# Kernel tuning notes

Measured on AMD Instinct MI355X. Metric: run time of the kernel, lower is better.

Reference implementation:

```python
import jax, jax.numpy as jnp
import numpy as np

V_NUM = 4
NUM_HEADS = 8


def setup_inputs() -> dict:
    key = jax.random.key(0)
    k1, k2, k3 = jax.random.split(key, 3)
    B, C, H, W = 8, 512, 24, 24
    x = jax.random.normal(k1, (B, C, H, W), dtype=jnp.float32)
    # 1x1 conv weights stored as [out_ch, in_ch]
    w_qkv = jax.random.normal(k2, (3 * C, C), dtype=jnp.float32) * (C ** -0.5)
    w_proj = jax.random.normal(k3, (C, C), dtype=jnp.float32) * (C ** -0.5)
    b_proj = jnp.zeros((C,), dtype=jnp.float32)
    return {"x": x, "w_qkv": w_qkv, "w_proj": w_proj, "b_proj": b_proj}


def reference(x, w_qkv, w_proj, b_proj):
    B, C, H, W = x.shape
    hd = C // NUM_HEADS          # head dim
    scale = hd ** -0.5
    g = B // V_NUM               # batch groups
    N = V_NUM * H * W            # tokens per group

    # 1x1 conv qkv (no bias): [B, 3C, H, W]
    qkv = jnp.einsum('bchw,oc->bohw', x, w_qkv)
    # [g, v, 3C, H, W] -> [g, 3C, v, H, W] -> [g, heads, 3*hd, N]
    t = qkv.reshape(g, V_NUM, 3 * C, H, W).transpose(0, 2, 1, 3, 4)
    t = t.reshape(g, NUM_HEADS, 3 * hd, N)
    q, k, v = jnp.split(t, 3, axis=2)  # each [g, heads, hd, N]

    # attn = k^T @ q * scale : [g, heads, N, N]
    attn = jnp.einsum('ghdn,ghdm->ghnm', k, q) * scale
    attn = jax.nn.softmax(attn, axis=-2)  # softmax over the k axis (dim=-2)

    # out = v @ attn : [g, heads, hd, N]
    out = jnp.einsum('ghdn,ghnm->ghdm', v, attn)
    # [g, C, v, H, W] -> [g, v, C, H, W] -> [B, C, H, W]
    out = out.reshape(g, C, V_NUM, H, W).transpose(0, 2, 1, 3, 4).reshape(B, C, H, W)

    # 1x1 conv proj with bias
    out = jnp.einsum('bchw,oc->bohw', out, w_proj) + b_proj[None, :, None, None]
    return out
```

## Files before the change

kernel.cpp:

```cpp
#include <hip/hip_runtime.h>
#include <stdint.h>

typedef _Float16 f16;
typedef _Float16 half8 __attribute__((ext_vector_type(8)));
typedef _Float16 half4 __attribute__((ext_vector_type(4)));
typedef float floatx4 __attribute__((ext_vector_type(4)));

#define LOG2E 1.44269504088896340736f

__device__ __forceinline__ void async_cp16(const void* g, void* l) {
  __builtin_amdgcn_global_load_lds((const __attribute__((address_space(1))) void*)g,
                                   (__attribute__((address_space(3))) void*)l, 16, 0, 0);
}

__global__ __launch_bounds__(256) void k_prep(const float* __restrict__ x,
                                              f16* __restrict__ XT,
                                              const float* __restrict__ wqkv,
                                              const float* __restrict__ wproj,
                                              f16* __restrict__ WQ, f16* __restrict__ WP) {
  __shared__ f16 sT[64][72];
  const int bid = blockIdx.x;
  const int tid = threadIdx.x;
  if (bid < 576) {
    const int hw0 = (bid % 9) * 64, c0 = ((bid / 9) & 7) * 64, b = bid / 72;
    const int cc = tid >> 6, hwc = tid & 63;
    const float* xb = x + (size_t)b * 294912;
    for (int i = 0; i < 16; ++i) {
      int c = c0 + i * 4 + cc;
      sT[hwc][i * 4 + cc] = (f16)xb[c * 576 + hw0 + hwc];
    }
    __syncthreads();
    const int c_c = tid & 63, rr = tid >> 6;
    f16* xtb = XT + ((size_t)b * 576 + hw0) * 512 + c0;
    for (int j = 0; j < 16; ++j) {
      int r = j * 4 + rr;
      xtb[(size_t)r * 512 + c_c] = sT[r][c_c];
    }
  } else {
    const float SCALE_Q = 0.125f * LOG2E;
    const int total1 = 1536 * 512, total2 = 512 * 512;
    for (int idx = (bid - 576) * 256 + tid; idx < total1 + total2; idx += 128 * 256) {
      if (idx < total1) {
        int row = idx >> 9;
        float v = wqkv[idx];
        if ((row % 192) < 64) v *= SCALE_Q;
        WQ[idx] = (f16)v;
      } else {
        WP[idx - total1] = (f16)wproj[idx - total1];
      }
    }
  }
}

__global__ __launch_bounds__(256) void k_qkv_gemm(const f16* __restrict__ XT,
                                                  const f16* __restrict__ WQ,
                                                  f16* __restrict__ Qh, f16* __restrict__ Kh,
                                                  f16* __restrict__ Vh) {
  const int t0 = blockIdx.x * 128, n0 = blockIdx.y * 128;
  __shared__ alignas(16) f16 smem[2 * 128 * 64];
  f16* sA = smem;
  f16* sB = smem + 128 * 64;
  const int tid = threadIdx.x;
  const int wave = tid >> 6, lane = tid & 63, quad = lane >> 4, l16 = lane & 15;
  const int msub = (wave & 1) * 64, nsub = (wave >> 1) * 64;
  const floatx4 fzero = {0.f, 0.f, 0.f, 0.f};
  floatx4 acc[4][4];
  for (int i = 0; i < 4; ++i)
    for (int j = 0; j < 4; ++j) acc[i][j] = fzero;

  for (int k0 = 0; k0 < 512; k0 += 64) {
    __syncthreads();
    for (int p = 0; p < 4; ++p) {
      int e = p * 256 + tid;
      int row = e >> 3, colb = e & 7;
      async_cp16((const char*)XT + ((size_t)(t0 + row) * 512 + k0 + colb * 8) * 2,
                 (char*)sA + e * 16);
      async_cp16((const char*)WQ + ((size_t)(n0 + row) * 512 + k0 + colb * 8) * 2,
                 (char*)sB + e * 16);
    }
    __syncthreads();
    for (int f = 0; f < 2; ++f) {
      half8 a[4], bfr[4];
      for (int ms = 0; ms < 4; ++ms)
        a[ms] = *(const half8*)&sA[(msub + ms * 16 + l16) * 64 + f * 32 + quad * 8];
      for (int ns = 0; ns < 4; ++ns)
        bfr[ns] = *(const half8*)&sB[(nsub + ns * 16 + l16) * 64 + f * 32 + quad * 8];
      for (int ms = 0; ms < 4; ++ms)
        for (int ns = 0; ns < 4; ++ns)
          acc[ms][ns] =
              __builtin_amdgcn_mfma_f32_16x16x32_f16(a[ms], bfr[ns], acc[ms][ns], 0, 0, 0);
    }
  }
  for (int ms = 0; ms < 4; ++ms) {
    int tbase = t0 + msub + ms * 16 + quad * 4;
    for (int ns = 0; ns < 4; ++ns) {
      int row = n0 + nsub + ns * 16 + l16;
      int h = row / 192, rr2 = row % 192;
      int sel = rr2 >> 6, d = rr2 & 63;
      if (sel == 2) continue;
      for (int r = 0; r < 4; ++r) {
        int t = tbase + r;
        int b = t / 576, hw = t % 576;
        int g = b >> 2, v = b & 3;
        int n = v * 576 + hw;
        int gh = g * 8 + h;
        f16 hv = (f16)acc[ms][ns][r];
        size_t idx = ((size_t)gh * 2304 + n) * 64 + d;
        if (sel == 0)
          Qh[idx] = hv;
        else
          Kh[idx] = hv;
      }
    }
  }
  const int r0 = n0 % 192;
  if (r0 != 0) {
    const int vloc = (r0 == 128) ? 0 : 64;
    const int h = (n0 + vloc) / 192;
    f16* sVT = smem;
    __syncthreads();
    if ((wave >> 1) == (vloc >> 6)) {
      for (int ms = 0; ms < 4; ++ms) {
        int tok = msub + ms * 16 + quad * 4;
        for (int ns = 0; ns < 4; ++ns) {
          int d = ns * 16 + l16;
          half4 hv;
          for (int r = 0; r < 4; ++r) hv[r] = (f16)acc[ms][ns][r];
          *(half4*)&sVT[d * 136 + tok] = hv;
        }
      }
    }
    __syncthreads();
    for (int pss = 0; pss < 4; ++pss) {
      int d = pss * 16 + (tid >> 4), chunk = tid & 15;
      int t = t0 + chunk * 8;
      int b = t / 576, hw = t - b * 576;
      int gh = (b >> 2) * 8 + h, n = (b & 3) * 576 + hw;
      *(half8*)(Vh + (size_t)gh * 147456 + (size_t)d * 2304 + n) =
          *(const half8*)&sVT[d * 136 + chunk * 8];
    }
  }
}

__global__ __launch_bounds__(384) void k_attn(const f16* __restrict__ Qh,
                                              const f16* __restrict__ Kh,
                                              const f16* __restrict__ Vh,
                                              f16* __restrict__ AOT) {
  const int mt = blockIdx.x, gh = blockIdx.y;
  const int m0 = mt * 48;
  const int g = gh >> 3, h = gh & 7;
  const f16* Qg = Qh + (size_t)gh * 147456;
  const f16* Kg = Kh + (size_t)gh * 147456;
  const f16* Vg = Vh + (size_t)gh * 147456;
  __shared__ alignas(16) f16 smem[16384];
  f16* sK = smem;
  f16* sV = smem + 8192;
  const int tid = threadIdx.x;
  const int wave = tid >> 6, lane = tid & 63, quad = lane >> 4, l16 = lane & 15;
  const int str = wave & 1, qgrp = wave >> 1;
  const floatx4 fzero = {0.f, 0.f, 0.f, 0.f};
  const int sw = l16 & 7;
  const int vsw = (l16 >> 1) & 3;

  auto stage_kv = [&](int ktile, int buf) {
#pragma unroll
    for (int p = 0; p < 3; ++p) {
      int idx = p * 384 + tid;
      if (idx < 1024) {
        int isV = idx >= 512;
        int rem = idx & 511;
        int st = rem >> 8, unit = rem & 255;
        if (!isV) {
          int row = unit >> 3, cb = unit & 7;
          async_cp16(
              Kg + (size_t)(st * 1152 + ktile * 32 + row) * 64 + ((cb ^ (row & 7)) << 3),
              (char*)(sK + (st * 2 + buf) * 2048) + unit * 16);
        } else {
          int row = unit >> 2, cb = unit & 3;
          async_cp16(Vg + (size_t)row * 2304 + st * 1152 + ktile * 32 +
                         ((cb ^ ((row >> 1) & 3)) << 3),
                     (char*)(sV + (st * 2 + buf) * 2048) + unit * 16);
        }
      }
    }
  };

  half8 qa[2];
  {
    int qrow = m0 + qgrp * 16 + l16;
    qa[0] = *(const half8*)(Qg + (size_t)qrow * 64 + quad * 8);
    qa[1] = *(const half8*)(Qg + (size_t)qrow * 64 + 32 + quad * 8);
  }

  stage_kv(0, 0);
  __syncthreads();
  stage_kv(1, 1);

  float l_lane = 0.f;
  floatx4 o[4];
  for (int dt = 0; dt < 4; ++dt) o[dt] = fzero;

  for (int kt = 0; kt < 36; ++kt) {
    const f16* bK = sK + (str * 2 + (kt & 1)) * 2048;
    const f16* bV = sV + (str * 2 + (kt & 1)) * 2048;

    half4 pf[2];
#pragma unroll
    for (int nt = 0; nt < 2; ++nt) {
      int krow = nt * 16 + l16;
      half8 kb0 = *(const half8*)&bK[krow * 64 + ((quad ^ sw) << 3)];
      half8 kb1 = *(const half8*)&bK[krow * 64 + (((4 + quad) ^ sw) << 3)];
      floatx4 t = __builtin_amdgcn_mfma_f32_16x16x32_f16(kb0, qa[0], fzero, 0, 0, 0);
      t = __builtin_amdgcn_mfma_f32_16x16x32_f16(kb1, qa[1], t, 0, 0, 0);
#pragma unroll
      for (int r = 0; r < 4; ++r) {
        float e = __builtin_amdgcn_exp2f(t[r]);
        l_lane += e;
        pf[nt][r] = (f16)e;
      }
    }
#pragma unroll
    for (int dt = 0; dt < 4; ++dt) {
      int vrow = dt * 16 + l16;
#pragma unroll
      for (int nt = 0; nt < 2; ++nt) {
        int chunk = nt * 2 + (quad >> 1);
        half4 vb = *(const half4*)&bV[vrow * 32 + ((chunk ^ vsw) << 3) + (quad & 1) * 4];
        o[dt] = __builtin_amdgcn_mfma_f32_16x16x16f16(pf[nt], vb, o[dt], 0, 0, 0);
      }
    }

    if (kt < 35) {
      __syncthreads();
      if (kt + 2 < 36) stage_kv(kt + 2, kt & 1);
    }
  }

  __syncthreads();
  float* cO = (float*)smem;
  float* cL = (float*)(smem + 8192);
  if (str == 1) {
    cL[qgrp * 64 + lane] = l_lane;
#pragma unroll
    for (int dt = 0; dt < 4; ++dt)
      *(floatx4*)&cO[((qgrp * 4 + dt) * 64 + lane) * 4] = o[dt];
  }
  __syncthreads();
  if (str == 0) {
    l_lane += cL[qgrp * 64 + lane];
#pragma unroll
    for (int dt = 0; dt < 4; ++dt)
      o[dt] += *(const floatx4*)&cO[((qgrp * 4 + dt) * 64 + lane) * 4];

    l_lane += __shfl_xor(l_lane, 16, 64);
    l_lane += __shfl_xor(l_lane, 32, 64);
    float inv[4];
#pragma unroll
    for (int r = 0; r < 4; ++r) {
      float lr = __shfl(l_lane, quad * 4 + r, 64);
      inv[r] = 1.f / lr;
    }
#pragma unroll
    for (int dt = 0; dt < 4; ++dt)
#pragma unroll
      for (int r = 0; r < 4; ++r) {
        int n_tok = m0 + qgrp * 16 + quad * 4 + r;
        int v = n_tok / 576, hw = n_tok % 576;
        int bb = g * 4 + v;
        int c = h * 64 + dt * 16 + l16;
        AOT[((size_t)bb * 576 + hw) * 512 + c] = (f16)(o[dt][r] * inv[r]);
      }
  }
}

__global__ __launch_bounds__(256) void k_proj_gemm(const f16* __restrict__ AOT,
                                                   const f16* __restrict__ WP,
                                                   const float* __restrict__ bias,
                                                   float* __restrict__ out) {
  const int o0 = blockIdx.x * 64, t0 = blockIdx.y * 128;
  __shared__ alignas(16) f16 sA[64 * 64];
  __shared__ alignas(16) f16 sB[128 * 64];
  const int tid = threadIdx.x;
  const int wave = tid >> 6, lane = tid & 63, quad = lane >> 4, l16 = lane & 15;
  const int msub = (wave & 1) * 32, nsub = (wave >> 1) * 64;
  const floatx4 fzero = {0.f, 0.f, 0.f, 0.f};
  floatx4 acc[2][4];
  for (int i = 0; i < 2; ++i)
    for (int j = 0; j < 4; ++j) acc[i][j] = fzero;

  for (int k0 = 0; k0 < 512; k0 += 64) {
    __syncthreads();
    for (int p = 0; p < 2; ++p) {
      int e = p * 256 + tid;
      int row = e >> 3, colb = e & 7;
      async_cp16((const char*)WP + ((size_t)(o0 + row) * 512 + k0 + colb * 8) * 2,
                 (char*)sA + e * 16);
    }
    for (int p = 0; p < 4; ++p) {
      int e = p * 256 + tid;
      int row = e >> 3, colb = e & 7;
      async_cp16((const char*)AOT + ((size_t)(t0 + row) * 512 + k0 + colb * 8) * 2,
                 (char*)sB + e * 16);
    }
    __syncthreads();
    for (int f = 0; f < 2; ++f) {
      half8 a[2], bfr[4];
      for (int ms = 0; ms < 2; ++ms)
        a[ms] = *(const half8*)&sA[(msub + ms * 16 + l16) * 64 + f * 32 + quad * 8];
      for (int ns = 0; ns < 4; ++ns)
        bfr[ns] = *(const half8*)&sB[(nsub + ns * 16 + l16) * 64 + f * 32 + quad * 8];
      for (int ms = 0; ms < 2; ++ms)
        for (int ns = 0; ns < 4; ++ns)
          acc[ms][ns] =
              __builtin_amdgcn_mfma_f32_16x16x32_f16(a[ms], bfr[ns], acc[ms][ns], 0, 0, 0);
    }
  }
  for (int ms = 0; ms < 2; ++ms) {
    int o_row = o0 + msub + ms * 16 + quad * 4;
    for (int ns = 0; ns < 4; ++ns) {
      int t = t0 + nsub + ns * 16 + l16;
      int b = t / 576, hw = t % 576;
      for (int r = 0; r < 4; ++r) {
        int orow = o_row + r;
        out[(size_t)b * 294912 + (size_t)orow * 576 + hw] = acc[ms][ns][r] + bias[orow];
      }
    }
  }
}

extern "C" void kernel_launch(void* const* d_in, const int* in_sizes, int n_in,
                              void* d_out, int out_size, void* d_ws, size_t ws_size,
                              hipStream_t stream) {
  const float* x = (const float*)d_in[0];
  const float* wqkv = (const float*)d_in[1];
  const float* wproj = (const float*)d_in[2];
  const float* bias = (const float*)d_in[3];
  float* out = (float*)d_out;
  char* ws = (char*)d_ws;
  f16* XT = (f16*)(ws + 0);
  f16* WQ = (f16*)(ws + 4718592);
  f16* WP = (f16*)(ws + 6291456);
  f16* Qh = (f16*)(ws + 6815744);
  f16* Kh = (f16*)(ws + 11534336);
  f16* Vh = (f16*)(ws + 16252928);
  f16* AOT = (f16*)(ws + 20971520);

  k_prep<<<dim3(704), dim3(256), 0, stream>>>(x, XT, wqkv, wproj, WQ, WP);
  k_qkv_gemm<<<dim3(36, 12), dim3(256), 0, stream>>>(XT, WQ, Qh, Kh, Vh);
  k_attn<<<dim3(48, 16), dim3(384), 0, stream>>>(Qh, Kh, Vh, AOT);
  k_proj_gemm<<<dim3(8, 36), dim3(256), 0, stream>>>(AOT, WP, bias, out);
}
```

Measured before the change: 148.0 us.

## Interleave V layout and load V directly from global into 16x16x32 MFMA

The V-producing kernel now writes V in an interleaved token order so that each lane can read a contiguous half8 of V straight from global memory. The attention kernel drops LDS staging for V, halves its shared memory, and raises launch bounds to ask for more resident blocks. The two P tiles are packed into one half8 so the PV product uses 16x16x32 MFMAs instead of pairs of 16x16x16. The exp results are converted with packed round-toward-zero and summed with fdot2. The risk is that direct global V loads expose latency that the async LDS pipeline used to hide, and the cL offset now depends on the reduced shared-memory layout.

```diff
diff --git a/kernel.cpp b/kernel.cpp
--- a/kernel.cpp
+++ b/kernel.cpp
@@ -4,6 +4,7 @@
 typedef _Float16 f16;
 typedef _Float16 half8 __attribute__((ext_vector_type(8)));
 typedef _Float16 half4 __attribute__((ext_vector_type(4)));
+typedef _Float16 half2 __attribute__((ext_vector_type(2)));
 typedef float floatx4 __attribute__((ext_vector_type(4)));
 
 #define LOG2E 1.44269504088896340736f
@@ -11,6 +12,10 @@
 __device__ __forceinline__ void async_cp16(const void* g, void* l) {
   __builtin_amdgcn_global_load_lds((const __attribute__((address_space(1))) void*)g,
                                    (__attribute__((address_space(3))) void*)l, 16, 0, 0);
+}
+
+__device__ __forceinline__ half2 pkrtz(float a, float b) {
+  return __builtin_bit_cast(half2, __builtin_amdgcn_cvt_pkrtz(a, b));
 }
 
 __global__ __launch_bounds__(256) void k_prep(const float* __restrict__ x,
@@ -132,55 +137,48 @@
     }
     __syncthreads();
     for (int pss = 0; pss < 4; ++pss) {
-      int d = pss * 16 + (tid >> 4), chunk = tid & 15;
-      int t = t0 + chunk * 8;
+      int d = pss * 16 + (tid >> 4);
+      int sub = tid & 15, gg = sub >> 2, u = sub & 3;
+      int t = t0 + gg * 32;
       int b = t / 576, hw = t - b * 576;
-      int gh = (b >> 2) * 8 + h, n = (b & 3) * 576 + hw;
-      *(half8*)(Vh + (size_t)gh * 147456 + (size_t)d * 2304 + n) =
-          *(const half8*)&sVT[d * 136 + chunk * 8];
-    }
-  }
-}
-
-__global__ __launch_bounds__(384) void k_attn(const f16* __restrict__ Qh,
-                                              const f16* __restrict__ Kh,
-                                              const f16* __restrict__ Vh,
-                                              f16* __restrict__ AOT) {
+      int gh = (b >> 2) * 8 + h, nb = (b & 3) * 576 + hw;
+      half4 va = *(const half4*)&sVT[d * 136 + gg * 32 + u * 4];
+      half4 vb2 = *(const half4*)&sVT[d * 136 + gg * 32 + 16 + u * 4];
+      half8 w = __builtin_shufflevector(va, vb2, 0, 4, 1, 5, 2, 6, 3, 7);
+      *(half8*)(Vh + (size_t)gh * 147456 + (size_t)d * 2304 + nb + u * 8) = w;
+    }
+  }
+}
+
+__global__ __launch_bounds__(384, 8) void k_attn(const f16* __restrict__ Qh,
+                                                 const f16* __restrict__ Kh,
+                                                 const f16* __restrict__ Vh,
+                                                 f16* __restrict__ AOT) {
   const int mt = blockIdx.x, gh = blockIdx.y;
   const int m0 = mt * 48;
   const int g = gh >> 3, h = gh & 7;
   const f16* Qg = Qh + (size_t)gh * 147456;
   const f16* Kg = Kh + (size_t)gh * 147456;
   const f16* Vg = Vh + (size_t)gh * 147456;
-  __shared__ alignas(16) f16 smem[16384];
+  __shared__ alignas(16) f16 smem[8192];
   f16* sK = smem;
-  f16* sV = smem + 8192;
   const int tid = threadIdx.x;
   const int wave = tid >> 6, lane = tid & 63, quad = lane >> 4, l16 = lane & 15;
   const int str = wave & 1, qgrp = wave >> 1;
   const floatx4 fzero = {0.f, 0.f, 0.f, 0.f};
   const int sw = l16 & 7;
-  const int vsw = (l16 >> 1) & 3;
-
-  auto stage_kv = [&](int ktile, int buf) {
-#pragma unroll
-    for (int p = 0; p < 3; ++p) {
+  const half2 one2 = {(f16)1.f, (f16)1.f};
+
+  auto stage_k = [&](int ktile, int buf) {
+#pragma unroll
+    for (int p = 0; p < 2; ++p) {
       int idx = p * 384 + tid;
-      if (idx < 1024) {
-        int isV = idx >= 512;
-        int rem = idx & 511;
-        int st = rem >> 8, unit = rem & 255;
-        if (!isV) {
-          int row = unit >> 3, cb = unit & 7;
-          async_cp16(
-              Kg + (size_t)(st * 1152 + ktile * 32 + row) * 64 + ((cb ^ (row & 7)) << 3),
-              (char*)(sK + (st * 2 + buf) * 2048) + unit * 16);
-        } else {
-          int row = unit >> 2, cb = unit & 3;
-          async_cp16(Vg + (size_t)row * 2304 + st * 1152 + ktile * 32 +
-                         ((cb ^ ((row >> 1) & 3)) << 3),
-                     (char*)(sV + (st * 2 + buf) * 2048) + unit * 16);
-        }
+      if (idx < 512) {
+        int st = idx >> 8, unit = idx & 255;
+        int row = unit >> 3, cb = unit & 7;
+        async_cp16(
+            Kg + (size_t)(st * 1152 + ktile * 32 + row) * 64 + ((cb ^ (row & 7)) << 3),
+            (char*)(sK + (st * 2 + buf) * 2048) + unit * 16);
       }
     }
   };
@@ -192,53 +190,63 @@
     qa[1] = *(const half8*)(Qg + (size_t)qrow * 64 + 32 + quad * 8);
   }
 
-  stage_kv(0, 0);
+  stage_k(0, 0);
   __syncthreads();
-  stage_kv(1, 1);
+  stage_k(1, 1);
 
   float l_lane = 0.f;
   floatx4 o[4];
   for (int dt = 0; dt < 4; ++dt) o[dt] = fzero;
 
+  const f16* Vbase = Vg + str * 1152;
+
   for (int kt = 0; kt < 36; ++kt) {
     const f16* bK = sK + (str * 2 + (kt & 1)) * 2048;
-    const f16* bV = sV + (str * 2 + (kt & 1)) * 2048;
-
-    half4 pf[2];
-#pragma unroll
-    for (int nt = 0; nt < 2; ++nt) {
-      int krow = nt * 16 + l16;
-      half8 kb0 = *(const half8*)&bK[krow * 64 + ((quad ^ sw) << 3)];
-      half8 kb1 = *(const half8*)&bK[krow * 64 + (((4 + quad) ^ sw) << 3)];
-      floatx4 t = __builtin_amdgcn_mfma_f32_16x16x32_f16(kb0, qa[0], fzero, 0, 0, 0);
-      t = __builtin_amdgcn_mfma_f32_16x16x32_f16(kb1, qa[1], t, 0, 0, 0);
-#pragma unroll
-      for (int r = 0; r < 4; ++r) {
-        float e = __builtin_amdgcn_exp2f(t[r]);
-        l_lane += e;
-        pf[nt][r] = (f16)e;
-      }
-    }
-#pragma unroll
-    for (int dt = 0; dt < 4; ++dt) {
-      int vrow = dt * 16 + l16;
-#pragma unroll
-      for (int nt = 0; nt < 2; ++nt) {
-        int chunk = nt * 2 + (quad >> 1);
-        half4 vb = *(const half4*)&bV[vrow * 32 + ((chunk ^ vsw) << 3) + (quad & 1) * 4];
-        o[dt] = __builtin_amdgcn_mfma_f32_16x16x16f16(pf[nt], vb, o[dt], 0, 0, 0);
-      }
-    }
+    const f16* vp = Vbase + kt * 32;
+
+    half8 vb[4];
+#pragma unroll
+    for (int dt = 0; dt < 4; ++dt)
+      vb[dt] = *(const half8*)(vp + (size_t)(dt * 16 + l16) * 2304 + quad * 8);
+
+    floatx4 ta, tb;
+    {
+      half8 k0 = *(const half8*)&bK[l16 * 64 + ((quad ^ sw) << 3)];
+      half8 k1 = *(const half8*)&bK[l16 * 64 + (((4 + quad) ^ sw) << 3)];
+      ta = __builtin_amdgcn_mfma_f32_16x16x32_f16(k0, qa[0], fzero, 0, 0, 0);
+      ta = __builtin_amdgcn_mfma_f32_16x16x32_f16(k1, qa[1], ta, 0, 0, 0);
+    }
+    {
+      half8 k0 = *(const half8*)&bK[(16 + l16) * 64 + ((quad ^ sw) << 3)];
+      half8 k1 = *(const half8*)&bK[(16 + l16) * 64 + (((4 + quad) ^ sw) << 3)];
+      tb = __builtin_amdgcn_mfma_f32_16x16x32_f16(k0, qa[0], fzero, 0, 0, 0);
+      tb = __builtin_amdgcn_mfma_f32_16x16x32_f16(k1, qa[1], tb, 0, 0, 0);
+    }
+    half2 a0 = pkrtz(__builtin_amdgcn_exp2f(ta[0]), __builtin_amdgcn_exp2f(ta[1]));
+    half2 a1 = pkrtz(__builtin_amdgcn_exp2f(ta[2]), __builtin_amdgcn_exp2f(ta[3]));
+    half2 b0 = pkrtz(__builtin_amdgcn_exp2f(tb[0]), __builtin_amdgcn_exp2f(tb[1]));
+    half2 b1 = pkrtz(__builtin_amdgcn_exp2f(tb[2]), __builtin_amdgcn_exp2f(tb[3]));
+    l_lane = __builtin_amdgcn_fdot2(a0, one2, l_lane, false);
+    l_lane = __builtin_amdgcn_fdot2(a1, one2, l_lane, false);
+    l_lane = __builtin_amdgcn_fdot2(b0, one2, l_lane, false);
+    l_lane = __builtin_amdgcn_fdot2(b1, one2, l_lane, false);
+    half4 pa = __builtin_shufflevector(a0, a1, 0, 1, 2, 3);
+    half4 pb = __builtin_shufflevector(b0, b1, 0, 1, 2, 3);
+    half8 pf = __builtin_shufflevector(pa, pb, 0, 4, 1, 5, 2, 6, 3, 7);
+
+#pragma unroll
+    for (int dt = 0; dt < 4; ++dt)
+      o[dt] = __builtin_amdgcn_mfma_f32_16x16x32_f16(pf, vb[dt], o[dt], 0, 0, 0);
 
     if (kt < 35) {
       __syncthreads();
-      if (kt + 2 < 36) stage_kv(kt + 2, kt & 1);
+      if (kt + 2 < 36) stage_k(kt + 2, kt & 1);
     }
   }
 
   __syncthreads();
   float* cO = (float*)smem;
-  float* cL = (float*)(smem + 8192);
+  float* cL = (float*)((char*)smem + 12288);
   if (str == 1) {
     cL[qgrp * 64 + lane] = l_lane;
 #pragma unroll
```

After: 191.8 us. +29.5%, slower.
